# Performance work log

Hardware: AMD Instinct MI355X
Metric: run time of the kernel (lower is better)

The kernel has to match this reference:

```python
import jax, jax.numpy as jnp
import numpy as np

D_DEC = 256  # decoder_size; W columns are [decoder | encoder] per the torch concat order


def setup_inputs() -> dict:
    key = jax.random.key(0)
    k1, k2, k3, k4 = jax.random.split(key, 4)
    B, S, E, D, A = 32, 4096, 256, 256, 256
    decoder_hidden = jax.random.normal(k1, (1, B, D), dtype=jnp.float32)
    encoder_outputs = jax.random.normal(k2, (S, B, E), dtype=jnp.float32)
    W = jax.random.normal(k3, (A, D + E), dtype=jnp.float32) / np.sqrt(D + E)
    b = jax.random.normal(k4, (A,), dtype=jnp.float32) * 0.02
    return {"decoder_hidden": decoder_hidden, "encoder_outputs": encoder_outputs, "W": W, "b": b}


def reference(decoder_hidden, encoder_outputs, W, b):
    # decoder_hidden: [1,B,D] -> [B,D]; encoder_outputs: [S,B,E] -> [B,S,E]
    dh = decoder_hidden[0]
    eo = jnp.transpose(encoder_outputs, (1, 0, 2))
    # Split the concat-linear: cat([dec, enc]) @ W.T == dec @ Wd.T + enc @ We.T
    Wd, We = W[:, :D_DEC], W[:, D_DEC:]
    # scores: tanh(linear) summed over attn dim -> [B,S]
    proj = dh @ Wd.T + b  # [B,A]
    attn = jnp.tanh(proj[:, None, :] + jnp.einsum('bse,ae->bsa', eo, We))
    scores = jnp.sum(attn, axis=2)  # [B,S]
    attn_softmax = jax.nn.softmax(scores, axis=1)  # [B,S]
    attended = jnp.einsum('bs,bse->be', attn_softmax, eo)  # [B,E]
    encoder_norms = jnp.linalg.norm(eo, axis=2)  # [B,S]
    attn_map = attn_softmax * encoder_norms
    return attended, attn_map
```

## Files before the change

kernel.cpp:

```cpp
#include <hip/hip_runtime.h>
#include <math.h>

#define B_  32
#define S_  4096
#define E_  256
#define A_  256
#define DE_ 512

typedef __attribute__((ext_vector_type(8))) short short8;
typedef __attribute__((ext_vector_type(4))) float f32x4;

__device__ inline unsigned short f2bf(float x) {
    unsigned int u = __float_as_uint(x);
    u += 0x7FFFu + ((u >> 16) & 1u);
    return (unsigned short)(u >> 16);
}
__device__ inline float tanh_fast(float x) {
    x = fminf(fmaxf(x, -15.f), 15.f);
    float t = __expf(2.f * x);
    return (t - 1.f) * __builtin_amdgcn_rcpf(t + 1.f);
}

__global__ __launch_bounds__(256) void prep_kernel(
    const float* __restrict__ W, const float* __restrict__ dh,
    const float* __restrict__ bias, unsigned short* __restrict__ wepk,
    float* __restrict__ proj, float* __restrict__ out)
{
    __shared__ float dh_lds[E_];
    const int bk  = blockIdx.x;
    const int tid = threadIdx.x;
    if (bk < 64) {
        const int idx = bk * 256 + tid;
        const int c     = idx >> 11;
        const int r     = idx & 2047;
        const int plane = r >> 10;
        const int kg    = (r >> 8) & 3;
        const int a     = r & 255;
        const float* src = W + (size_t)a * DE_ + E_ + c * 32 + kg * 8;
        unsigned int pk[4];
        #pragma unroll
        for (int j = 0; j < 4; ++j) {
            float x0 = src[2 * j], x1 = src[2 * j + 1];
            unsigned int u0 = __float_as_uint(x0) & 0xFFFF0000u;
            unsigned int u1 = __float_as_uint(x1) & 0xFFFF0000u;
            if (plane) {
                unsigned short l0 = f2bf(x0 - __uint_as_float(u0));
                unsigned short l1 = f2bf(x1 - __uint_as_float(u1));
                pk[j] = (unsigned int)l0 | ((unsigned int)l1 << 16);
            } else {
                pk[j] = (u0 >> 16) | u1;
            }
        }
        *(uint4*)&wepk[(size_t)idx * 8] = make_uint4(pk[0], pk[1], pk[2], pk[3]);
    } else if (bk < 96) {
        const int b = bk - 64;
        const int a = tid;
        dh_lds[a] = dh[b * E_ + a];
        __syncthreads();
        float acc = bias[a];
        const float* wrow = W + (size_t)a * DE_;
        #pragma unroll
        for (int d = 0; d < E_; d += 4) {
            float4 w = *(const float4*)(wrow + d);
            acc += dh_lds[d] * w.x + dh_lds[d+1] * w.y
                 + dh_lds[d+2] * w.z + dh_lds[d+3] * w.w;
        }
        proj[b * A_ + a] = acc;
    } else {
        #pragma unroll
        for (int j = tid; j < B_ * E_; j += 256) out[j] = 0.f;
    }
}

__global__ __launch_bounds__(256, 3) void scores_kernel(
    const float* __restrict__ eo, const unsigned short* __restrict__ wepk,
    const float* __restrict__ proj,
    float* __restrict__ scores, float* __restrict__ nsq)
{
    __shared__ __align__(16) unsigned char pool[18944];
    unsigned short* eo_hl = (unsigned short*)pool;

    const int tid = threadIdx.x;
    const int b   = blockIdx.x & (B_ - 1);
    const int s0  = (blockIdx.x >> 5) * 64;
    const int w   = tid >> 6, l = tid & 63;
    const int lq  = l >> 4,  lr = l & 15;

    const int erow = tid >> 2;
    const int ekg  = tid & 3;
    const float* ebase = eo + (size_t)(s0 + erow) * (B_ * E_) + b * E_ + ekg * 8;

    const int wunit = lq * 256 + w * 64 + lr;

    f32x4 acc[4][4];
    #pragma unroll
    for (int i = 0; i < 4; ++i)
        #pragma unroll
        for (int j = 0; j < 4; ++j)
            acc[i][j] = (f32x4){0.f, 0.f, 0.f, 0.f};
    float nacc = 0.f;

    float4 ea0 = *(const float4*)(ebase);
    float4 ea1 = *(const float4*)(ebase + 4);

    for (int c = 0; c < 8; ++c) {
        __syncthreads();
        short8 bh[4], bl[4];
        {
            const unsigned short* wsrc = wepk + (size_t)(c * 2048 + wunit) * 8;
            #pragma unroll
            for (int nt = 0; nt < 4; ++nt) {
                bh[nt] = *(const short8*)(wsrc + (size_t)(nt * 16) * 8);
                bl[nt] = *(const short8*)(wsrc + (size_t)(1024 + nt * 16) * 8);
            }
        }
        {
            float4 v0 = ea0;
            float4 v1 = ea1;
            nacc += v0.x*v0.x + v0.y*v0.y + v0.z*v0.z + v0.w*v0.w
                  + v1.x*v1.x + v1.y*v1.y + v1.z*v1.z + v1.w*v1.w;
            float xs[8] = {v0.x, v0.y, v0.z, v0.w, v1.x, v1.y, v1.z, v1.w};
            unsigned int hp[4], lp[4];
            #pragma unroll
            for (int j = 0; j < 4; ++j) {
                unsigned int u0 = __float_as_uint(xs[2*j])   & 0xFFFF0000u;
                unsigned int u1 = __float_as_uint(xs[2*j+1]) & 0xFFFF0000u;
                hp[j] = (u0 >> 16) | u1;
                lp[j] = (unsigned int)f2bf(xs[2*j]   - __uint_as_float(u0))
                      | ((unsigned int)f2bf(xs[2*j+1] - __uint_as_float(u1)) << 16);
            }
            const int u = ekg * 66 + erow;
            *(uint4*)&eo_hl[(size_t)u * 8]         = make_uint4(hp[0], hp[1], hp[2], hp[3]);
            *(uint4*)&eo_hl[(size_t)(264 + u) * 8] = make_uint4(lp[0], lp[1], lp[2], lp[3]);
        }
        __syncthreads();
        if (c < 7) {
            ea0 = *(const float4*)(ebase + (c + 1) * 32);
            ea1 = *(const float4*)(ebase + (c + 1) * 32 + 4);
        }
        #pragma unroll
        for (int mt = 0; mt < 4; ++mt) {
            const int au = lq * 66 + mt * 16 + lr;
            short8 ah = *(const short8*)&eo_hl[(size_t)au * 8];
            short8 al = *(const short8*)&eo_hl[(size_t)(264 + au) * 8];
            #pragma unroll
            for (int nt = 0; nt < 4; ++nt) {
                acc[mt][nt] = __builtin_amdgcn_mfma_f32_16x16x32_bf16(ah, bh[nt], acc[mt][nt], 0, 0, 0);
                acc[mt][nt] = __builtin_amdgcn_mfma_f32_16x16x32_bf16(ah, bl[nt], acc[mt][nt], 0, 0, 0);
                acc[mt][nt] = __builtin_amdgcn_mfma_f32_16x16x32_bf16(al, bh[nt], acc[mt][nt], 0, 0, 0);
            }
        }
    }
    __syncthreads();

    float* red4  = (float*)pool;
    float* npart = (float*)(pool + 16896);
    float* qpart = (float*)(pool + 17920);
    float pr[4];
    #pragma unroll
    for (int nt = 0; nt < 4; ++nt) pr[nt] = proj[b * A_ + w * 64 + nt * 16 + lr];
    #pragma unroll
    for (int mt = 0; mt < 4; ++mt) {
        #pragma unroll
        for (int r = 0; r < 4; ++r) {
            float s = 0.f;
            #pragma unroll
            for (int nt = 0; nt < 4; ++nt)
                s += tanh_fast(pr[nt] + acc[mt][nt][r]);
            red4[(w * 16 + lr) * 66 + (mt * 16 + lq * 4 + r)] = s;
        }
    }
    npart[tid] = nacc;
    __syncthreads();
    {
        const int row = tid >> 2, quarter = tid & 3;
        float s = 0.f;
        #pragma unroll
        for (int j = 0; j < 16; ++j) s += red4[(quarter * 16 + j) * 66 + row];
        qpart[quarter * 64 + row] = s;
    }
    __syncthreads();
    if (tid < 64) {
        scores[b * S_ + s0 + tid] = qpart[tid] + qpart[64 + tid]
                                  + qpart[128 + tid] + qpart[192 + tid];
        nsq[b * S_ + s0 + tid] = npart[4 * tid] + npart[4 * tid + 1]
                               + npart[4 * tid + 2] + npart[4 * tid + 3];
    }
}

__global__ __launch_bounds__(256) void stats_kernel(
    const float* __restrict__ scores, float* __restrict__ nsq_pv,
    float* __restrict__ out)
{
    __shared__ float red[256];
    const int tid  = threadIdx.x;
    const int b    = blockIdx.x & (B_ - 1);
    const int part = blockIdx.x >> 5;
    float v[16];
    float m = -1e30f;
    #pragma unroll
    for (int i = 0; i < 16; ++i) {
        v[i] = scores[b * S_ + i * 256 + tid];
        m = fmaxf(m, v[i]);
    }
    red[tid] = m;
    __syncthreads();
    for (int off = 128; off > 0; off >>= 1) {
        if (tid < off) red[tid] = fmaxf(red[tid], red[tid + off]);
        __syncthreads();
    }
    m = red[0];
    __syncthreads();
    float sum = 0.f;
    #pragma unroll
    for (int i = 0; i < 16; ++i) sum += __expf(v[i] - m);
    red[tid] = sum;
    __syncthreads();
    for (int off = 128; off > 0; off >>= 1) {
        if (tid < off) red[tid] += red[tid + off];
        __syncthreads();
    }
    const float inv = 1.f / red[0];
    #pragma unroll
    for (int j = 0; j < 2; ++j) {
        const int i = part * 2 + j;
        const int s = i * 256 + tid;
        const float pv = __expf(v[i] - m) * inv;
        out[B_ * E_ + b * S_ + s] = pv * sqrtf(nsq_pv[b * S_ + s]);
        nsq_pv[b * S_ + s] = pv;
    }
}

__global__ __launch_bounds__(256) void attend_kernel(
    const float* __restrict__ eo, const float* __restrict__ pv,
    float* __restrict__ out)
{
    __shared__ float4 acc_red[4][64];
    const int tid = threadIdx.x;
    const int b   = blockIdx.x & (B_ - 1);
    const int ch  = blockIdx.x / B_;
    const int le = tid & 63, sg = tid >> 6;
    const int s0 = ch * 128 + sg * 32;
    float4 a = make_float4(0.f, 0.f, 0.f, 0.f);
    #pragma unroll 8
    for (int s = 0; s < 32; ++s) {
        float p = pv[b * S_ + s0 + s];
        float4 e = *(const float4*)(eo + (size_t)(s0 + s) * (B_ * E_)
                                       + b * E_ + le * 4);
        a.x = fmaf(p, e.x, a.x);
        a.y = fmaf(p, e.y, a.y);
        a.z = fmaf(p, e.z, a.z);
        a.w = fmaf(p, e.w, a.w);
    }
    acc_red[sg][le] = a;
    __syncthreads();
    if (tid < 64) {
        float4 a0 = acc_red[0][tid], a1 = acc_red[1][tid];
        float4 a2 = acc_red[2][tid], a3 = acc_red[3][tid];
        float* dst = out + b * E_ + tid * 4;
        atomicAdd(dst + 0, a0.x + a1.x + a2.x + a3.x);
        atomicAdd(dst + 1, a0.y + a1.y + a2.y + a3.y);
        atomicAdd(dst + 2, a0.z + a1.z + a2.z + a3.z);
        atomicAdd(dst + 3, a0.w + a1.w + a2.w + a3.w);
    }
}

extern "C" void kernel_launch(void* const* d_in, const int* in_sizes, int n_in,
                              void* d_out, int out_size, void* d_ws, size_t ws_size,
                              hipStream_t stream)
{
    const float* dh   = (const float*)d_in[0];
    const float* eo   = (const float*)d_in[1];
    const float* W    = (const float*)d_in[2];
    const float* bias = (const float*)d_in[3];
    float* out = (float*)d_out;
    float* ws  = (float*)d_ws;

    float* projb  = ws;
    float* nsqb   = ws + 8192;
    float* scores = nsqb + S_ * B_;
    unsigned short* wepk = (unsigned short*)(scores + S_ * B_);

    prep_kernel   <<<97,              256, 0, stream>>>(W, dh, bias, wepk, projb, out);
    scores_kernel <<<B_ * (S_ / 64),  256, 0, stream>>>(eo, wepk, projb, scores, nsqb);
    stats_kernel  <<<B_ * 8,          256, 0, stream>>>(scores, nsqb, out);
    attend_kernel <<<B_ * (S_ / 128), 256, 0, stream>>>(eo, nsqb, out);
}
```

Measured before the change: 256.8 us.

## Load encoder tiles directly into MFMA A-fragments, removing LDS staging and barriers

Each wave now reads its own encoder rows from global memory straight into registers laid out as MFMA A operands, and does the bf16 hi/lo split in registers. This drops the shared-memory staging buffer and both per-chunk __syncthreads. The cost is that all four waves redundantly load and convert the same 64x32 encoder tile, roughly four times the global/L2 read traffic and conversion ALU work. The software prefetch of the next chunk is also gone. Norm partials are now taken only from wave 0, with the final reduction indexing changed to match.

```diff
diff --git a/kernel.cpp b/kernel.cpp
--- a/kernel.cpp
+++ b/kernel.cpp
@@ -78,7 +78,6 @@
     float* __restrict__ scores, float* __restrict__ nsq)
 {
     __shared__ __align__(16) unsigned char pool[18944];
-    unsigned short* eo_hl = (unsigned short*)pool;
 
     const int tid = threadIdx.x;
     const int b   = blockIdx.x & (B_ - 1);
@@ -86,11 +85,8 @@
     const int w   = tid >> 6, l = tid & 63;
     const int lq  = l >> 4,  lr = l & 15;
 
-    const int erow = tid >> 2;
-    const int ekg  = tid & 3;
-    const float* ebase = eo + (size_t)(s0 + erow) * (B_ * E_) + b * E_ + ekg * 8;
-
     const int wunit = lq * 256 + w * 64 + lr;
+    const float* esrc = eo + (size_t)(s0 + lr) * (B_ * E_) + b * E_ + lq * 8;
 
     f32x4 acc[4][4];
     #pragma unroll
@@ -98,13 +94,16 @@
         #pragma unroll
         for (int j = 0; j < 4; ++j)
             acc[i][j] = (f32x4){0.f, 0.f, 0.f, 0.f};
-    float nacc = 0.f;
-
-    float4 ea0 = *(const float4*)(ebase);
-    float4 ea1 = *(const float4*)(ebase + 4);
+    float nacc[4] = {0.f, 0.f, 0.f, 0.f};
 
     for (int c = 0; c < 8; ++c) {
-        __syncthreads();
+        float4 r0[4], r1[4];
+        #pragma unroll
+        for (int mt = 0; mt < 4; ++mt) {
+            const float* p = esrc + (size_t)(mt * 16) * (B_ * E_) + c * 32;
+            r0[mt] = *(const float4*)(p);
+            r1[mt] = *(const float4*)(p + 4);
+        }
         short8 bh[4], bl[4];
         {
             const unsigned short* wsrc = wepk + (size_t)(c * 2048 + wunit) * 8;
@@ -114,44 +113,29 @@
                 bl[nt] = *(const short8*)(wsrc + (size_t)(1024 + nt * 16) * 8);
             }
         }
-        {
-            float4 v0 = ea0;
-            float4 v1 = ea1;
-            nacc += v0.x*v0.x + v0.y*v0.y + v0.z*v0.z + v0.w*v0.w
-                  + v1.x*v1.x + v1.y*v1.y + v1.z*v1.z + v1.w*v1.w;
-            float xs[8] = {v0.x, v0.y, v0.z, v0.w, v1.x, v1.y, v1.z, v1.w};
-            unsigned int hp[4], lp[4];
+        #pragma unroll
+        for (int mt = 0; mt < 4; ++mt) {
+            float xs[8] = {r0[mt].x, r0[mt].y, r0[mt].z, r0[mt].w,
+                           r1[mt].x, r1[mt].y, r1[mt].z, r1[mt].w};
+            nacc[mt] += xs[0]*xs[0] + xs[1]*xs[1] + xs[2]*xs[2] + xs[3]*xs[3]
+                      + xs[4]*xs[4] + xs[5]*xs[5] + xs[6]*xs[6] + xs[7]*xs[7];
+            union { short8 s; unsigned int u[4]; } ah, al;
             #pragma unroll
             for (int j = 0; j < 4; ++j) {
                 unsigned int u0 = __float_as_uint(xs[2*j])   & 0xFFFF0000u;
                 unsigned int u1 = __float_as_uint(xs[2*j+1]) & 0xFFFF0000u;
-                hp[j] = (u0 >> 16) | u1;
-                lp[j] = (unsigned int)f2bf(xs[2*j]   - __uint_as_float(u0))
-                      | ((unsigned int)f2bf(xs[2*j+1] - __uint_as_float(u1)) << 16);
-            }
-            const int u = ekg * 66 + erow;
-            *(uint4*)&eo_hl[(size_t)u * 8]         = make_uint4(hp[0], hp[1], hp[2], hp[3]);
-            *(uint4*)&eo_hl[(size_t)(264 + u) * 8] = make_uint4(lp[0], lp[1], lp[2], lp[3]);
-        }
-        __syncthreads();
-        if (c < 7) {
-            ea0 = *(const float4*)(ebase + (c + 1) * 32);
-            ea1 = *(const float4*)(ebase + (c + 1) * 32 + 4);
-        }
-        #pragma unroll
-        for (int mt = 0; mt < 4; ++mt) {
-            const int au = lq * 66 + mt * 16 + lr;
-            short8 ah = *(const short8*)&eo_hl[(size_t)au * 8];
-            short8 al = *(const short8*)&eo_hl[(size_t)(264 + au) * 8];
+                ah.u[j] = (u0 >> 16) | u1;
+                al.u[j] = (unsigned int)f2bf(xs[2*j]   - __uint_as_float(u0))
+                        | ((unsigned int)f2bf(xs[2*j+1] - __uint_as_float(u1)) << 16);
+            }
             #pragma unroll
             for (int nt = 0; nt < 4; ++nt) {
-                acc[mt][nt] = __builtin_amdgcn_mfma_f32_16x16x32_bf16(ah, bh[nt], acc[mt][nt], 0, 0, 0);
-                acc[mt][nt] = __builtin_amdgcn_mfma_f32_16x16x32_bf16(ah, bl[nt], acc[mt][nt], 0, 0, 0);
-                acc[mt][nt] = __builtin_amdgcn_mfma_f32_16x16x32_bf16(al, bh[nt], acc[mt][nt], 0, 0, 0);
-            }
-        }
-    }
-    __syncthreads();
+                acc[mt][nt] = __builtin_amdgcn_mfma_f32_16x16x32_bf16(ah.s, bh[nt], acc[mt][nt], 0, 0, 0);
+                acc[mt][nt] = __builtin_amdgcn_mfma_f32_16x16x32_bf16(ah.s, bl[nt], acc[mt][nt], 0, 0, 0);
+                acc[mt][nt] = __builtin_amdgcn_mfma_f32_16x16x32_bf16(al.s, bh[nt], acc[mt][nt], 0, 0, 0);
+            }
+        }
+    }
 
     float* red4  = (float*)pool;
     float* npart = (float*)(pool + 16896);
@@ -170,7 +154,10 @@
             red4[(w * 16 + lr) * 66 + (mt * 16 + lq * 4 + r)] = s;
         }
     }
-    npart[tid] = nacc;
+    if (w == 0) {
+        #pragma unroll
+        for (int mt = 0; mt < 4; ++mt) npart[mt * 64 + l] = nacc[mt];
+    }
     __syncthreads();
     {
         const int row = tid >> 2, quarter = tid & 3;
@@ -183,8 +170,9 @@
     if (tid < 64) {
         scores[b * S_ + s0 + tid] = qpart[tid] + qpart[64 + tid]
                                   + qpart[128 + tid] + qpart[192 + tid];
-        nsq[b * S_ + s0 + tid] = npart[4 * tid] + npart[4 * tid + 1]
-                               + npart[4 * tid + 2] + npart[4 * tid + 3];
+        const int mt = tid >> 4, lr2 = tid & 15;
+        nsq[b * S_ + s0 + tid] = npart[mt * 64 + lr2]      + npart[mt * 64 + 16 + lr2]
+                               + npart[mt * 64 + 32 + lr2] + npart[mt * 64 + 48 + lr2];
     }
 }
 
```

New measurement: 321.5 us. +25.2%, slower.

## Double-buffer the encoder LDS tile to drop one barrier per chunk

Applied to the files above, without the earlier changes.

The scores kernel now splits its shared-memory staging area into two buffers and software-pipelines the K loop. While the MFMAs consume the current chunk, the next chunk's fp32-to-bf16 hi/lo conversion is written into the other buffer, and the chunk after that is prefetched from global memory. This removes one __syncthreads per iteration and overlaps the conversion with the matrix work. In exchange it holds more live registers (extra A fragments and prefetched values), which could hurt scheduling under the 3-blocks-per-CU launch bound.

```diff
diff --git a/kernel.cpp b/kernel.cpp
--- a/kernel.cpp
+++ b/kernel.cpp
@@ -19,6 +19,26 @@
     x = fminf(fmaxf(x, -15.f), 15.f);
     float t = __expf(2.f * x);
     return (t - 1.f) * __builtin_amdgcn_rcpf(t + 1.f);
+}
+
+__device__ __forceinline__ void conv_write(float4 v0, float4 v1,
+                                           unsigned short* buf, int eu,
+                                           float& nacc)
+{
+    nacc += v0.x*v0.x + v0.y*v0.y + v0.z*v0.z + v0.w*v0.w
+          + v1.x*v1.x + v1.y*v1.y + v1.z*v1.z + v1.w*v1.w;
+    float xs[8] = {v0.x, v0.y, v0.z, v0.w, v1.x, v1.y, v1.z, v1.w};
+    unsigned int hp[4], lp[4];
+    #pragma unroll
+    for (int j = 0; j < 4; ++j) {
+        unsigned int u0 = __float_as_uint(xs[2*j])   & 0xFFFF0000u;
+        unsigned int u1 = __float_as_uint(xs[2*j+1]) & 0xFFFF0000u;
+        hp[j] = (u0 >> 16) | u1;
+        lp[j] = (unsigned int)f2bf(xs[2*j]   - __uint_as_float(u0))
+              | ((unsigned int)f2bf(xs[2*j+1] - __uint_as_float(u1)) << 16);
+    }
+    *(uint4*)&buf[(size_t)eu * 8]         = make_uint4(hp[0], hp[1], hp[2], hp[3]);
+    *(uint4*)&buf[(size_t)(264 + eu) * 8] = make_uint4(lp[0], lp[1], lp[2], lp[3]);
 }
 
 __global__ __launch_bounds__(256) void prep_kernel(
@@ -89,6 +109,7 @@
     const int erow = tid >> 2;
     const int ekg  = tid & 3;
     const float* ebase = eo + (size_t)(s0 + erow) * (B_ * E_) + b * E_ + ekg * 8;
+    const int eu = ekg * 66 + erow;
 
     const int wunit = lq * 256 + w * 64 + lr;
 
@@ -100,11 +121,24 @@
             acc[i][j] = (f32x4){0.f, 0.f, 0.f, 0.f};
     float nacc = 0.f;
 
-    float4 ea0 = *(const float4*)(ebase);
-    float4 ea1 = *(const float4*)(ebase + 4);
+    float pr[4];
+    #pragma unroll
+    for (int nt = 0; nt < 4; ++nt) pr[nt] = proj[b * A_ + w * 64 + nt * 16 + lr];
+
+    {
+        float4 v0 = *(const float4*)(ebase);
+        float4 v1 = *(const float4*)(ebase + 4);
+        conv_write(v0, v1, eo_hl, eu, nacc);
+    }
+    float4 va0 = *(const float4*)(ebase + 32);
+    float4 va1 = *(const float4*)(ebase + 36);
+    __syncthreads();
 
     for (int c = 0; c < 8; ++c) {
-        __syncthreads();
+        const int p = c & 1;
+        unsigned short* rb = eo_hl + (size_t)p * 528 * 8;
+        unsigned short* wb = eo_hl + (size_t)(1 - p) * 528 * 8;
+
         short8 bh[4], bl[4];
         {
             const unsigned short* wsrc = wepk + (size_t)(c * 2048 + wunit) * 8;
@@ -114,51 +148,46 @@
                 bl[nt] = *(const short8*)(wsrc + (size_t)(1024 + nt * 16) * 8);
             }
         }
-        {
-            float4 v0 = ea0;
-            float4 v1 = ea1;
-            nacc += v0.x*v0.x + v0.y*v0.y + v0.z*v0.z + v0.w*v0.w
-                  + v1.x*v1.x + v1.y*v1.y + v1.z*v1.z + v1.w*v1.w;
-            float xs[8] = {v0.x, v0.y, v0.z, v0.w, v1.x, v1.y, v1.z, v1.w};
-            unsigned int hp[4], lp[4];
-            #pragma unroll
-            for (int j = 0; j < 4; ++j) {
-                unsigned int u0 = __float_as_uint(xs[2*j])   & 0xFFFF0000u;
-                unsigned int u1 = __float_as_uint(xs[2*j+1]) & 0xFFFF0000u;
-                hp[j] = (u0 >> 16) | u1;
-                lp[j] = (unsigned int)f2bf(xs[2*j]   - __uint_as_float(u0))
-                      | ((unsigned int)f2bf(xs[2*j+1] - __uint_as_float(u1)) << 16);
-            }
-            const int u = ekg * 66 + erow;
-            *(uint4*)&eo_hl[(size_t)u * 8]         = make_uint4(hp[0], hp[1], hp[2], hp[3]);
-            *(uint4*)&eo_hl[(size_t)(264 + u) * 8] = make_uint4(lp[0], lp[1], lp[2], lp[3]);
-        }
-        __syncthreads();
-        if (c < 7) {
-            ea0 = *(const float4*)(ebase + (c + 1) * 32);
-            ea1 = *(const float4*)(ebase + (c + 1) * 32 + 4);
-        }
-        #pragma unroll
-        for (int mt = 0; mt < 4; ++mt) {
+        short8 ah[2], al[2];
+        #pragma unroll
+        for (int mt = 0; mt < 2; ++mt) {
             const int au = lq * 66 + mt * 16 + lr;
-            short8 ah = *(const short8*)&eo_hl[(size_t)au * 8];
-            short8 al = *(const short8*)&eo_hl[(size_t)(264 + au) * 8];
+            ah[mt] = *(const short8*)&rb[(size_t)au * 8];
+            al[mt] = *(const short8*)&rb[(size_t)(264 + au) * 8];
+        }
+        if (c < 7) conv_write(va0, va1, wb, eu, nacc);
+        if (c < 6) {
+            va0 = *(const float4*)(ebase + (c + 2) * 32);
+            va1 = *(const float4*)(ebase + (c + 2) * 32 + 4);
+        }
+        #pragma unroll
+        for (int mt = 0; mt < 2; ++mt) {
             #pragma unroll
             for (int nt = 0; nt < 4; ++nt) {
-                acc[mt][nt] = __builtin_amdgcn_mfma_f32_16x16x32_bf16(ah, bh[nt], acc[mt][nt], 0, 0, 0);
-                acc[mt][nt] = __builtin_amdgcn_mfma_f32_16x16x32_bf16(ah, bl[nt], acc[mt][nt], 0, 0, 0);
-                acc[mt][nt] = __builtin_amdgcn_mfma_f32_16x16x32_bf16(al, bh[nt], acc[mt][nt], 0, 0, 0);
+                acc[mt][nt] = __builtin_amdgcn_mfma_f32_16x16x32_bf16(ah[mt], bh[nt], acc[mt][nt], 0, 0, 0);
+                acc[mt][nt] = __builtin_amdgcn_mfma_f32_16x16x32_bf16(ah[mt], bl[nt], acc[mt][nt], 0, 0, 0);
+                acc[mt][nt] = __builtin_amdgcn_mfma_f32_16x16x32_bf16(al[mt], bh[nt], acc[mt][nt], 0, 0, 0);
             }
         }
+        #pragma unroll
+        for (int mt = 2; mt < 4; ++mt) {
+            const int au = lq * 66 + mt * 16 + lr;
+            short8 ah2 = *(const short8*)&rb[(size_t)au * 8];
+            short8 al2 = *(const short8*)&rb[(size_t)(264 + au) * 8];
+            #pragma unroll
+            for (int nt = 0; nt < 4; ++nt) {
+                acc[mt][nt] = __builtin_amdgcn_mfma_f32_16x16x32_bf16(ah2, bh[nt], acc[mt][nt], 0, 0, 0);
+                acc[mt][nt] = __builtin_amdgcn_mfma_f32_16x16x32_bf16(ah2, bl[nt], acc[mt][nt], 0, 0, 0);
+                acc[mt][nt] = __builtin_amdgcn_mfma_f32_16x16x32_bf16(al2, bh[nt], acc[mt][nt], 0, 0, 0);
+            }
+        }
+        if (c < 7) __syncthreads();
     }
     __syncthreads();
 
     float* red4  = (float*)pool;
     float* npart = (float*)(pool + 16896);
     float* qpart = (float*)(pool + 17920);
-    float pr[4];
-    #pragma unroll
-    for (int nt = 0; nt < 4; ++nt) pr[nt] = proj[b * A_ + w * 64 + nt * 16 + lr];
     #pragma unroll
     for (int mt = 0; mt < 4; ++mt) {
         #pragma unroll
```

New measurement: 259.6 us. No clear change (+1.1%).
